# Kernel optimization log

Hardware: AMD Instinct MI355X
Metric: run time of the kernel (lower is better)

Reference implementation:

```python
import jax, jax.numpy as jnp
import numpy as np

jax.config.update("jax_enable_x64", True)  # I-BERT's FixedPointMul runs in double precision

# I-BERT IntSoftmax constants
COEF0 = 0.35815147
COEF1 = 0.96963238 / COEF0
COEF2 = 1.0 / COEF0
X0 = -0.6931          # -ln(2)
N_EXP = 30            # large integer n in int_exp
MAX_BIT = 32
OUTPUT_BIT = 8
ACT_BIT = 16

B, H, S = 1, 12, 2048


def sg(x):
    return jax.lax.stop_gradient(x)


def ste_round(x):
    # straight-through round (matches torch round_ste / SymmetricQuantFunction backward)
    return x + sg(jnp.round(x) - x)


def ste_floor(x):
    return x + sg(jnp.floor(x) - x)


def sym_scale(x_min, x_max, bits):
    # symmetric_linear_quantization_params: scale = clamp(max(|min|,|max|),1e-8)/(2^(b-1)-1)
    n = 2 ** (bits - 1) - 1
    s = jnp.maximum(jnp.abs(x_min), jnp.abs(x_max))
    return sg(jnp.maximum(s, 1e-8) / n)


def fixedpoint_mul(pre_act, pre_sf, z_sf, bits):
    # I-BERT fixedpoint_mul: requantize pre_act (granularity pre_sf) to scale z_sf
    # using a 31-bit mantissa frexp decomposition, computed in float64.
    n = 2 ** (bits - 1) - 1
    z_int = ste_round(pre_act.astype(jnp.float64) / pre_sf.astype(jnp.float64))
    new_scale = sg((pre_sf / z_sf).astype(jnp.float64))
    e = jnp.floor(jnp.log2(jnp.abs(new_scale))) + 1.0   # frexp exponent
    m_int = jnp.round((new_scale / 2.0 ** e) * 2.0 ** 31)  # 31-bit mantissa
    out = ste_round(z_int * m_int / 2.0 ** (31.0 - e))
    return jnp.clip(out, -n - 1, n).astype(jnp.float32)


def quant_softmax(x):
    n16 = 2 ** (ACT_BIT - 1) - 1
    # ---- outer QuantAct(16, symmetric), specified min/max = data min/max ----
    sf = sym_scale(sg(x.min()), sg(x.max()), ACT_BIT)
    x_int = jnp.clip(ste_round(x / sf), -n16 - 1, n16)
    quant_x = x_int * sf  # dequantized activation returned by QuantAct
    # ---- IntSoftmax ----
    xi = quant_x / sf
    xi = xi - xi.max(axis=-1, keepdims=True)
    # int_exp: shift-based exponential, exp(x) = 2^(-q) * exp(r), r in (-ln2, 0]
    x0_int = sg(jnp.floor(X0 / sf))               # negative integer
    xi = jnp.maximum(xi, N_EXP * x0_int)
    q = ste_floor(xi / x0_int)
    r = xi - x0_int * q
    # int_polynomial: 2nd-order poly approximation of exp on (-ln2, 0]
    b_int = sg(jnp.floor(COEF1 / sf))
    c_int = sg(jnp.floor(COEF2 / sf ** 2))
    z = r * (r + b_int) + c_int
    exp_sf = sg(COEF0 * sf ** 2) / 2.0 ** N_EXP
    exp_int = jnp.maximum(ste_floor(z * 2.0 ** (N_EXP - q)), 0.0)
    # ---- inner QuantAct(16): requantize exp to 16 bits to avoid overflow ----
    act_sf = sym_scale(sg(exp_int.min()), sg(exp_int.max()), ACT_BIT)
    exp_int16 = fixedpoint_mul(exp_int, exp_sf, act_sf, ACT_BIT)
    # ---- integer normalization to output_bit fixed point ----
    s = exp_int16.sum(axis=-1, keepdims=True)
    factor = ste_floor(2.0 ** MAX_BIT / s)
    out_int = ste_floor(exp_int16 * factor / 2.0 ** (MAX_BIT - OUTPUT_BIT))
    out_sf = 1.0 / 2.0 ** OUTPUT_BIT
    return out_int * out_sf  # softmax probs quantized to 1/256 grid


def setup_inputs() -> dict:
    key = jax.random.key(0)
    x = jax.random.normal(key, (B, H, S, S), dtype=jnp.float32)
    return {"x": x}


def reference(x):
    return quant_softmax(x)
```

## Files before the change

kernel.cpp:

```cpp
#include <hip/hip_runtime.h>
#include <math.h>


#define ROW_S 2048
#define MM_BLOCKS 2048

typedef float floatx4 __attribute__((ext_vector_type(4)));

struct Scalars {
    double exp_sf_d;
    double inv_exp_sf;
    double m_int;
    double inv_pow;
    float  sf;
    float  inv_sf;
    float  x0_int;
    float  inv_x0;
    float  b_int;
    float  c_int;
    float  thirty_x0;
    float  _pad;
};

__device__ __forceinline__ float div_rn(float a, float b, float inv) {
    const float q0 = __fmul_rn(a, inv);
    const float r  = __fmaf_rn(-b, q0, a);
    return __fmaf_rn(r, inv, q0);
}
__device__ __forceinline__ double ddiv_rn(double a, double b, double inv) {
    const double q0 = __dmul_rn(a, inv);
    const double r  = __fma_rn(-b, q0, a);
    return __fma_rn(r, inv, q0);
}

__global__ __launch_bounds__(256) void k_amax(const float* __restrict__ x,
                                              unsigned* __restrict__ amax_bits,
                                              unsigned* __restrict__ counter,
                                              Scalars* __restrict__ sc,
                                              int n4) {
    const int tid = threadIdx.x;
    float am = 0.0f;
    const float4* x4 = (const float4*)x;
    for (int i = blockIdx.x * 256 + tid; i < n4; i += MM_BLOCKS * 256) {
        float4 v = x4[i];
        am = fmaxf(am, fabsf(v.x));
        am = fmaxf(am, fabsf(v.y));
        am = fmaxf(am, fabsf(v.z));
        am = fmaxf(am, fabsf(v.w));
    }
#pragma unroll
    for (int m = 32; m > 0; m >>= 1) am = fmaxf(am, __shfl_xor(am, m));
    __shared__ float sred[4];
    const int wave = tid >> 6, lane = tid & 63;
    if (lane == 0) sred[wave] = am;
    __syncthreads();
    if (tid == 0) {
        const float ba = fmaxf(fmaxf(sred[0], sred[1]), fmaxf(sred[2], sred[3]));
        atomicMax(amax_bits, __float_as_uint(ba));
        __threadfence();
        const unsigned old = atomicAdd(counter, 1u);
        if (old == MM_BLOCKS - 1) {
            const float sabs = __uint_as_float(atomicMax(amax_bits, 0u));
            const float sf    = __fdiv_rn(fmaxf(sabs, 1e-8f), 32767.0f);
            const float x0i   = floorf(__fdiv_rn((float)(-0.6931), sf));
            const float sfsq  = __fmul_rn(sf, sf);
            const float b_int = floorf(__fdiv_rn((float)(0.96963238 / 0.35815147), sf));
            const float c_int = floorf(__fdiv_rn((float)(1.0 / 0.35815147), sfsq));
            const float exp_sf = __fdiv_rn(__fmul_rn((float)(0.35815147), sfsq), 1073741824.0f);
            const float emax   = __fmul_rn(c_int, 1073741824.0f);
            const float act_sf = __fdiv_rn(fmaxf(emax, 1e-8f), 32767.0f);
            const float  nsf = __fdiv_rn(exp_sf, act_sf);
            const double ns  = (double)nsf;
            int E;
            (void)frexp(ns, &E);
            const double m_int = rint(ldexp(ns, 31 - E));
            sc->exp_sf_d   = (double)exp_sf;
            sc->inv_exp_sf = 1.0 / (double)exp_sf;
            sc->m_int      = m_int;
            sc->inv_pow    = ldexp(1.0, E - 31);
            sc->sf         = sf;
            sc->inv_sf     = __fdiv_rn(1.0f, sf);
            sc->x0_int     = x0i;
            sc->inv_x0     = __fdiv_rn(1.0f, x0i);
            sc->b_int      = b_int;
            sc->c_int      = c_int;
            sc->thirty_x0  = __fmul_rn(30.0f, x0i);
        }
    }
}

__global__ __launch_bounds__(256) void k_row(const float* __restrict__ x,
                                             float* __restrict__ out,
                                             const Scalars* __restrict__ scp) {
    const int lane = threadIdx.x & 63;
    const int wave = threadIdx.x >> 6;
    const size_t row = (size_t)blockIdx.x * 4 + wave;
    const floatx4* x4 = (const floatx4*)(x + row * ROW_S);
    floatx4* o4 = (floatx4*)(out + row * ROW_S);

    floatx4 v[8];
#pragma unroll
    for (int i = 0; i < 8; ++i) v[i] = x4[i * 64 + lane];

    const Scalars sc = *scp;
    const float sf = sc.sf, inv_sf = sc.inv_sf;

    float rmax = -INFINITY;
#pragma unroll
    for (int i = 0; i < 8; ++i) {
#pragma unroll
        for (int c = 0; c < 4; ++c) rmax = fmaxf(rmax, v[i][c]);
    }
#pragma unroll
    for (int m = 32; m > 0; m >>= 1) rmax = fmaxf(rmax, __shfl_xor(rmax, m));

    float t = rintf(div_rn(rmax, sf, inv_sf));
    t = fminf(fmaxf(t, -32768.0f), 32767.0f);
    t = __fmul_rn(t, sf);
    const float ximax = div_rn(t, sf, inv_sf);

    float ssum = 0.0f;
#pragma unroll
    for (int i = 0; i < 8; ++i) {
#pragma unroll
        for (int c = 0; c < 4; ++c) {
            float q = rintf(div_rn(v[i][c], sf, inv_sf));
            q = fminf(fmaxf(q, -32768.0f), 32767.0f);
            q = __fmul_rn(q, sf);
            const float xi = div_rn(q, sf, inv_sf);
            const float xs = __fsub_rn(xi, ximax);
            const float xm = fmaxf(xs, sc.thirty_x0);
            const float qf = floorf(div_rn(xm, sc.x0_int, sc.inv_x0));
            const float r  = __fsub_rn(xm, __fmul_rn(sc.x0_int, qf));
            const float z  = __fadd_rn(__fmul_rn(r, __fadd_rn(r, sc.b_int)), sc.c_int);
            const int   qi = (int)qf;
            const float p2 = __int_as_float((157 - qi) << 23);
            const float ei = fmaxf(floorf(__fmul_rn(z, p2)), 0.0f);
            const double a  = (double)ei;
            const double zi = rint(ddiv_rn(a, sc.exp_sf_d, sc.inv_exp_sf));
            double ovd = rint(__dmul_rn(__dmul_rn(zi, sc.m_int), sc.inv_pow));
            ovd = fmin(fmax(ovd, -32768.0), 32767.0);
            const float e16 = (float)ovd;
            v[i][c] = e16;
            ssum += e16;
        }
    }
#pragma unroll
    for (int m = 32; m > 0; m >>= 1) ssum += __shfl_xor(ssum, m);
    const float factor = floorf(__fdiv_rn(4294967296.0f, ssum));

#pragma unroll
    for (int i = 0; i < 8; ++i) {
        floatx4 w;
#pragma unroll
        for (int c = 0; c < 4; ++c) {
            const float oi = floorf(__fmul_rn(__fmul_rn(v[i][c], factor), 5.9604644775390625e-8f));
            w[c] = __fmul_rn(oi, 0.00390625f);
        }
        __builtin_nontemporal_store(w, &o4[i * 64 + lane]);
    }
}

extern "C" void kernel_launch(void* const* d_in, const int* in_sizes, int n_in,
                              void* d_out, int out_size, void* d_ws, size_t ws_size,
                              hipStream_t stream) {
    const float* x = (const float*)d_in[0];
    float* out = (float*)d_out;
    const int n = in_sizes[0];
    const int rows = n / ROW_S;

    unsigned* amax_bits = (unsigned*)d_ws;
    unsigned* counter   = amax_bits + 1;
    Scalars*  sc        = (Scalars*)((char*)d_ws + 64);

    hipMemsetAsync(d_ws, 0, 8, stream);
    k_amax<<<MM_BLOCKS, 256, 0, stream>>>(x, amax_bits, counter, sc, n / 4);
    k_row<<<rows / 4, 256, 0, stream>>>(x, out, sc);
}
```

Measured before the change: 408.7 us.

## Replace atomic last-block amax reduction with per-block partials and scalar kernel

Removes the hipMemsetAsync and the atomicMax plus counter last-block pattern. Each block now writes its partial max to a workspace array, and a separate single-block kernel reduces the partials and computes the quantization scalars. The amax loop is also unrolled four ways to keep more loads in flight. This trades a memset and global atomics for an extra small kernel launch.

```diff
diff --git a/kernel.cpp b/kernel.cpp
--- a/kernel.cpp
+++ b/kernel.cpp
@@ -4,6 +4,7 @@
 
 #define ROW_S 2048
 #define MM_BLOCKS 2048
+#define MM_STRIDE (MM_BLOCKS * 256)
 
 typedef float floatx4 __attribute__((ext_vector_type(4)));
 
@@ -34,19 +35,26 @@
 }
 
 __global__ __launch_bounds__(256) void k_amax(const float* __restrict__ x,
-                                              unsigned* __restrict__ amax_bits,
-                                              unsigned* __restrict__ counter,
-                                              Scalars* __restrict__ sc,
+                                              float* __restrict__ pmax,
                                               int n4) {
     const int tid = threadIdx.x;
+    const float4* x4 = (const float4*)x;
     float am = 0.0f;
-    const float4* x4 = (const float4*)x;
-    for (int i = blockIdx.x * 256 + tid; i < n4; i += MM_BLOCKS * 256) {
-        float4 v = x4[i];
-        am = fmaxf(am, fabsf(v.x));
-        am = fmaxf(am, fabsf(v.y));
-        am = fmaxf(am, fabsf(v.z));
-        am = fmaxf(am, fabsf(v.w));
+    int i = blockIdx.x * 256 + tid;
+    for (; i + 3 * MM_STRIDE < n4; i += 4 * MM_STRIDE) {
+        const float4 v0 = x4[i];
+        const float4 v1 = x4[i + MM_STRIDE];
+        const float4 v2 = x4[i + 2 * MM_STRIDE];
+        const float4 v3 = x4[i + 3 * MM_STRIDE];
+        const float m0 = fmaxf(fmaxf(fabsf(v0.x), fabsf(v0.y)), fmaxf(fabsf(v0.z), fabsf(v0.w)));
+        const float m1 = fmaxf(fmaxf(fabsf(v1.x), fabsf(v1.y)), fmaxf(fabsf(v1.z), fabsf(v1.w)));
+        const float m2 = fmaxf(fmaxf(fabsf(v2.x), fabsf(v2.y)), fmaxf(fabsf(v2.z), fabsf(v2.w)));
+        const float m3 = fmaxf(fmaxf(fabsf(v3.x), fabsf(v3.y)), fmaxf(fabsf(v3.z), fabsf(v3.w)));
+        am = fmaxf(am, fmaxf(fmaxf(m0, m1), fmaxf(m2, m3)));
+    }
+    for (; i < n4; i += MM_STRIDE) {
+        const float4 v = x4[i];
+        am = fmaxf(am, fmaxf(fmaxf(fabsf(v.x), fabsf(v.y)), fmaxf(fabsf(v.z), fabsf(v.w))));
     }
 #pragma unroll
     for (int m = 32; m > 0; m >>= 1) am = fmaxf(am, __shfl_xor(am, m));
@@ -54,38 +62,47 @@
     const int wave = tid >> 6, lane = tid & 63;
     if (lane == 0) sred[wave] = am;
     __syncthreads();
+    if (tid == 0)
+        pmax[blockIdx.x] = fmaxf(fmaxf(sred[0], sred[1]), fmaxf(sred[2], sred[3]));
+}
+
+__global__ __launch_bounds__(256) void k_scalars(const float* __restrict__ pmax,
+                                                 Scalars* __restrict__ sc) {
+    const int tid = threadIdx.x;
+    float am = 0.0f;
+    for (int i = tid; i < MM_BLOCKS; i += 256) am = fmaxf(am, pmax[i]);
+#pragma unroll
+    for (int m = 32; m > 0; m >>= 1) am = fmaxf(am, __shfl_xor(am, m));
+    __shared__ float sred[4];
+    const int wave = tid >> 6, lane = tid & 63;
+    if (lane == 0) sred[wave] = am;
+    __syncthreads();
     if (tid == 0) {
-        const float ba = fmaxf(fmaxf(sred[0], sred[1]), fmaxf(sred[2], sred[3]));
-        atomicMax(amax_bits, __float_as_uint(ba));
-        __threadfence();
-        const unsigned old = atomicAdd(counter, 1u);
-        if (old == MM_BLOCKS - 1) {
-            const float sabs = __uint_as_float(atomicMax(amax_bits, 0u));
-            const float sf    = __fdiv_rn(fmaxf(sabs, 1e-8f), 32767.0f);
-            const float x0i   = floorf(__fdiv_rn((float)(-0.6931), sf));
-            const float sfsq  = __fmul_rn(sf, sf);
-            const float b_int = floorf(__fdiv_rn((float)(0.96963238 / 0.35815147), sf));
-            const float c_int = floorf(__fdiv_rn((float)(1.0 / 0.35815147), sfsq));
-            const float exp_sf = __fdiv_rn(__fmul_rn((float)(0.35815147), sfsq), 1073741824.0f);
-            const float emax   = __fmul_rn(c_int, 1073741824.0f);
-            const float act_sf = __fdiv_rn(fmaxf(emax, 1e-8f), 32767.0f);
-            const float  nsf = __fdiv_rn(exp_sf, act_sf);
-            const double ns  = (double)nsf;
-            int E;
-            (void)frexp(ns, &E);
-            const double m_int = rint(ldexp(ns, 31 - E));
-            sc->exp_sf_d   = (double)exp_sf;
-            sc->inv_exp_sf = 1.0 / (double)exp_sf;
-            sc->m_int      = m_int;
-            sc->inv_pow    = ldexp(1.0, E - 31);
-            sc->sf         = sf;
-            sc->inv_sf     = __fdiv_rn(1.0f, sf);
-            sc->x0_int     = x0i;
-            sc->inv_x0     = __fdiv_rn(1.0f, x0i);
-            sc->b_int      = b_int;
-            sc->c_int      = c_int;
-            sc->thirty_x0  = __fmul_rn(30.0f, x0i);
-        }
+        const float sabs = fmaxf(fmaxf(sred[0], sred[1]), fmaxf(sred[2], sred[3]));
+        const float sf    = __fdiv_rn(fmaxf(sabs, 1e-8f), 32767.0f);
+        const float x0i   = floorf(__fdiv_rn((float)(-0.6931), sf));
+        const float sfsq  = __fmul_rn(sf, sf);
+        const float b_int = floorf(__fdiv_rn((float)(0.96963238 / 0.35815147), sf));
+        const float c_int = floorf(__fdiv_rn((float)(1.0 / 0.35815147), sfsq));
+        const float exp_sf = __fdiv_rn(__fmul_rn((float)(0.35815147), sfsq), 1073741824.0f);
+        const float emax   = __fmul_rn(c_int, 1073741824.0f);
+        const float act_sf = __fdiv_rn(fmaxf(emax, 1e-8f), 32767.0f);
+        const float  nsf = __fdiv_rn(exp_sf, act_sf);
+        const double ns  = (double)nsf;
+        int E;
+        (void)frexp(ns, &E);
+        const double m_int = rint(ldexp(ns, 31 - E));
+        sc->exp_sf_d   = (double)exp_sf;
+        sc->inv_exp_sf = 1.0 / (double)exp_sf;
+        sc->m_int      = m_int;
+        sc->inv_pow    = ldexp(1.0, E - 31);
+        sc->sf         = sf;
+        sc->inv_sf     = __fdiv_rn(1.0f, sf);
+        sc->x0_int     = x0i;
+        sc->inv_x0     = __fdiv_rn(1.0f, x0i);
+        sc->b_int      = b_int;
+        sc->c_int      = c_int;
+        sc->thirty_x0  = __fmul_rn(30.0f, x0i);
     }
 }
 
@@ -169,11 +186,10 @@
     const int n = in_sizes[0];
     const int rows = n / ROW_S;
 
-    unsigned* amax_bits = (unsigned*)d_ws;
-    unsigned* counter   = amax_bits + 1;
-    Scalars*  sc        = (Scalars*)((char*)d_ws + 64);
+    Scalars* sc = (Scalars*)d_ws;
+    float* pmax = (float*)((char*)d_ws + 256);
 
-    hipMemsetAsync(d_ws, 0, 8, stream);
-    k_amax<<<MM_BLOCKS, 256, 0, stream>>>(x, amax_bits, counter, sc, n / 4);
+    k_amax<<<MM_BLOCKS, 256, 0, stream>>>(x, pmax, n / 4);
+    k_scalars<<<1, 256, 0, stream>>>(pmax, sc);
     k_row<<<rows / 4, 256, 0, stream>>>(x, out, sc);
 }
```

After: 357.8 us. 1.14x faster.
